# Optimization experiments

Measured on AMD Instinct MI355X. Metric: run time of the kernel, lower is better.

## Reference

```python
import jax, jax.numpy as jnp
import numpy as np

# 4x4 Walsh-Hadamard matrix in natural (Hadamard/Kronecker) order: H4 = H2 (x) H2
_H4 = jnp.array([[1, 1, 1, 1],
                 [1, -1, 1, -1],
                 [1, 1, -1, -1],
                 [1, -1, -1, 1]], dtype=jnp.float32)

T = 16          # number of 2D WHT coefficients (4x4 block)
BLK = 4         # spatial block size


def _iwht_stream(trans, weight):
    """trans: (16, B, nH, nW, C); weight: (16, C, K) -> out: (B, 4*nH, 4*nW, K).

    Per-coefficient channel mixing in the transform domain, then inverse 2D
    Walsh-Hadamard transform (separable, scale 1/16) back to spatial domain.
    """
    _, B, nH, nW, C = trans.shape
    K = weight.shape[2]
    # transform-domain channel mixing: (t,b,h,w,c) x (t,c,k) -> (t,b,h,w,k)
    mixed = jnp.einsum('tbhwc,tck->tbhwk', trans, weight)
    # split coefficient index t = 4*u + v (row/col frequency)
    mixed = mixed.reshape(BLK, BLK, B, nH, nW, K)
    # inverse separable WHT: out[b,nh,i,nw,j,k] = (1/16) sum_{u,v} H4[i,u] H4[j,v] mixed[u,v,...]
    out = jnp.einsum('iu,jv,uvbhwk->bhiwjk', _H4, _H4, mixed) * (1.0 / 16.0)
    return out.reshape(B, nH * BLK, nW * BLK, K)


def setup_inputs() -> dict:
    key = jax.random.key(0)
    k1, k2, k3, k4 = jax.random.split(key, 4)
    B, nH, nW, C = 16, 28, 28, 64
    out_channels = 128
    K1 = out_channels // 2
    K2 = out_channels // 2 + out_channels % 2
    transIm1 = jax.random.normal(k1, (T, B, nH, nW, C), dtype=jnp.float32)
    transIm2 = jax.random.normal(k2, (T, B, nH, nW, C), dtype=jnp.float32)
    weight1 = jax.random.normal(k3, (T, C, K1), dtype=jnp.float32) * 0.02
    weight2 = jax.random.normal(k4, (T, C, K2), dtype=jnp.float32) * 0.02
    bias1 = jnp.zeros((1, 1, 1, K1), dtype=jnp.float32)
    bias2 = jnp.zeros((1, 1, 1, K2), dtype=jnp.float32)
    return {"transIm1": transIm1, "transIm2": transIm2,
            "weight1": weight1, "weight2": weight2,
            "bias1": bias1, "bias2": bias2}


def reference(transIm1, transIm2, weight1, weight2, bias1, bias2):
    out1 = _iwht_stream(transIm1, weight1) + bias1
    out2 = _iwht_stream(transIm2, weight2) + bias2
    return (out1, out2)
```

## Files before the change

kernel.cpp:

```cpp
#include <hip/hip_runtime.h>
#include <hip/hip_bf16.h>

typedef float f32x4 __attribute__((ext_vector_type(4)));
typedef short s16x8 __attribute__((ext_vector_type(8)));

#define NPIX       12544
#define OUT_STRIDE 12845056
#define NTILES     1568
#define GRIDX      512

__device__ __forceinline__ unsigned short f2bf(float x) {
    union { float f; unsigned u; } un; un.f = x;
    unsigned r = un.u + 0x7FFFu + ((un.u >> 16) & 1u);
    return (unsigned short)(r >> 16);
}

__device__ __forceinline__ short bfs(float x) {
    __hip_bfloat16 h = __float2bfloat16(x);
    return *reinterpret_cast<short*>(&h);
}

__device__ __forceinline__ void gload_lds16(const void* g, void* l) {
    __builtin_amdgcn_global_load_lds(
        (const __attribute__((address_space(1))) unsigned int*)g,
        (__attribute__((address_space(3))) unsigned int*)l, 16, 0, 0);
}

__global__ __launch_bounds__(256) void repack_weights(
        const float* __restrict__ w1, const float* __restrict__ w2,
        unsigned short* __restrict__ wf) {
    int gid = blockIdx.x * 256 + threadIdx.x;
    int k = gid & 63;
    int c = (gid >> 6) & 63;
    int t = (gid >> 12) & 15;
    int s = (gid >> 16) & 1;
    const float* __restrict__ w = s ? w2 : w1;
    float val = w[gid & 65535] * 0.0625f;
    int e = c & 7, lhi = (c >> 3) & 3, ks = c >> 5;
    int l  = lhi * 16 + (k & 15);
    int nt = k >> 4;
    int dst = ((((s * 16 + t) * 2 + ks) * 4 + nt) * 64 + l) * 8 + e;
    wf[dst] = f2bf(val);
}

__global__ __launch_bounds__(256, 2) void iwht_main(
        const float* __restrict__ trans1, const float* __restrict__ trans2,
        const unsigned short* __restrict__ wf,
        const float* __restrict__ bias1, const float* __restrict__ bias2,
        float* __restrict__ out) {
    __shared__ __align__(16) unsigned char lds[65536];

    const int tid  = threadIdx.x;
    const int wid  = tid >> 6;
    const int lane = tid & 63;
    const int lrow = lane & 15;
    const int lhi  = lane >> 4;

    const s16x8* __restrict__ wbb = (const s16x8*)wf;

    for (int tau = blockIdx.x; tau < NTILES; tau += GRIDX) {
        const int s   = (tau >= 784) ? 1 : 0;
        const int bid = tau - s * 784;
        const float* __restrict__ trans = s ? trans2 : trans1;
        const int p0 = bid * 16;

        {
            const int ks = wid >> 1, j = wid & 1;
            const float* g0 = trans + (size_t)(p0 + lrow) * 64
                                    + (ks * 8 + lhi * 2 + j) * 4;
            #pragma unroll
            for (int t = 0; t < 16; ++t)
                gload_lds16(g0 + (size_t)t * (NPIX * 64),
                            lds + t * 4096 + wid * 1024);
        }

        const s16x8* __restrict__ wb = wbb + (size_t)s * 8192 + wid * 64 + lane;
        s16x8 bA[8], bB[8];
        #pragma unroll
        for (int v = 0; v < 4; ++v) {
            bA[v]     = wb[(size_t)(v * 8 + 0) * 64];
            bA[4 + v] = wb[(size_t)(v * 8 + 4) * 64];
        }

        f32x4 o[4][4];
        #pragma unroll
        for (int i = 0; i < 4; ++i)
            #pragma unroll
            for (int j = 0; j < 4; ++j)
                o[i][j] = (f32x4){0.f, 0.f, 0.f, 0.f};

        __syncthreads();

        #pragma unroll 1
        for (int uu = 0; uu < 4; uu += 2) {
            #pragma unroll
            for (int v = 0; v < 4; ++v) {
                int t = (uu + 1) * 4 + v;
                bB[v]     = wb[(size_t)(t * 8 + 0) * 64];
                bB[4 + v] = wb[(size_t)(t * 8 + 4) * 64];
            }
            #pragma unroll
            for (int half = 0; half < 2; ++half) {
                const int u = uu + half;
                f32x4 acc[4];
                #pragma unroll
                for (int v = 0; v < 4; ++v) {
                    const int t = u * 4 + v;
                    const unsigned char* ab = lds + t * 4096 + lane * 16;
                    f32x4 q0 = *(const f32x4*)(ab);
                    f32x4 q1 = *(const f32x4*)(ab + 1024);
                    f32x4 q2 = *(const f32x4*)(ab + 2048);
                    f32x4 q3 = *(const f32x4*)(ab + 3072);
                    s16x8 a0, a1;
                    #pragma unroll
                    for (int e = 0; e < 4; ++e) {
                        a0[e] = bfs(q0[e]); a0[4 + e] = bfs(q1[e]);
                        a1[e] = bfs(q2[e]); a1[4 + e] = bfs(q3[e]);
                    }
                    f32x4 tacc = {0.f, 0.f, 0.f, 0.f};
                    if (half == 0) {
                        tacc = __builtin_amdgcn_mfma_f32_16x16x32_bf16(a0, bA[v],     tacc, 0, 0, 0);
                        tacc = __builtin_amdgcn_mfma_f32_16x16x32_bf16(a1, bA[4 + v], tacc, 0, 0, 0);
                    } else {
                        tacc = __builtin_amdgcn_mfma_f32_16x16x32_bf16(a0, bB[v],     tacc, 0, 0, 0);
                        tacc = __builtin_amdgcn_mfma_f32_16x16x32_bf16(a1, bB[4 + v], tacc, 0, 0, 0);
                    }
                    acc[v] = tacc;
                }
                if (half == 0 && uu + 2 < 4) {
                    #pragma unroll
                    for (int v = 0; v < 4; ++v) {
                        int t = (uu + 2) * 4 + v;
                        bA[v]     = wb[(size_t)(t * 8 + 0) * 64];
                        bA[4 + v] = wb[(size_t)(t * 8 + 4) * 64];
                    }
                }
                f32x4 e0 = acc[0] + acc[1], e1 = acc[0] - acc[1];
                f32x4 e2 = acc[2] + acc[3], e3 = acc[2] - acc[3];
                f32x4 g0 = e0 + e2, g1 = e1 + e3, g2 = e0 - e2, g3 = e1 - e3;
                const float s1 = (u & 1) ? -1.f : 1.f;
                const float s2 = (u & 2) ? -1.f : 1.f;
                const float s3 = s1 * s2;
                #pragma unroll
                for (int j = 0; j < 4; ++j) {
                    f32x4 gj = (j == 0) ? g0 : ((j == 1) ? g1 : ((j == 2) ? g2 : g3));
                    o[0][j] += gj;
                    o[1][j] += s1 * gj;
                    o[2][j] += s2 * gj;
                    o[3][j] += s3 * gj;
                }
            }
        }

        const float* __restrict__ bias = s ? bias2 : bias1;
        const int k = wid * 16 + lrow;
        const float bk = bias[k];
        __syncthreads();
        #pragma unroll
        for (int i = 0; i < 4; ++i)
            #pragma unroll
            for (int j = 0; j < 4; ++j)
                #pragma unroll
                for (int r = 0; r < 4; ++r) {
                    int p = lhi * 4 + r;
                    int w = k ^ (4 * (p & 7)) ^ (16 * (j & 1));
                    *(float*)(lds + p * 4096 + i * 1024 + j * 256 + w * 4) = o[i][j][r] + bk;
                }
        __syncthreads();
        const int bimg = bid / 49;
        const int hw0  = (bid % 49) * 16;
        float* __restrict__ outp = out + (s ? (size_t)OUT_STRIDE : 0);
        #pragma unroll
        for (int n = 0; n < 16; ++n) {
            int idx = wid * 16 + n;
            int p = idx >> 2, i = idx & 3;
            int hw = hw0 + p;
            int h = hw / 28, w = hw % 28;
            size_t rowbase = ((size_t)(bimg * 112 + h * 4 + i) * 112 + w * 4) * 64;
            int g = (lane & 15) ^ (p & 7) ^ (4 * ((lane >> 4) & 1));
            f32x4 val = *(const f32x4*)(lds + p * 4096 + i * 1024
                                        + (lane >> 4) * 256 + g * 16);
            *(f32x4*)(outp + rowbase + lane * 4) = val;
        }
        __syncthreads();
    }
}

extern "C" void kernel_launch(void* const* d_in, const int* in_sizes, int n_in,
                              void* d_out, int out_size, void* d_ws, size_t ws_size,
                              hipStream_t stream) {
    const float* t1 = (const float*)d_in[0];
    const float* t2 = (const float*)d_in[1];
    const float* w1 = (const float*)d_in[2];
    const float* w2 = (const float*)d_in[3];
    const float* b1 = (const float*)d_in[4];
    const float* b2 = (const float*)d_in[5];
    unsigned short* wfrag = (unsigned short*)d_ws;
    float* out = (float*)d_out;

    repack_weights<<<dim3(512), dim3(256), 0, stream>>>(w1, w2, wfrag);
    iwht_main<<<dim3(GRIDX), dim3(256), 0, stream>>>(t1, t2, wfrag, b1, b2, out);
}
```

Measured before the change: 202.7 us.

## Double-buffer half-tile input staging and store output directly from registers

The per-tile loop is split into half-tiles of 8 WHT coefficients. Each half is staged into one of two LDS buffers while the previous half is computed, using an explicit vmcnt wait and a raw barrier in place of full __syncthreads. The LDS transpose of the output is removed: each lane writes its accumulated values straight to global memory as scalar stores, with bias values hoisted out of the loop. This aims to hide global load latency and cut LDS round trips and barriers. The cost is many more, narrower store instructions with less coalescing, and weight fragments reloaded for every half.

```diff
diff --git a/kernel.cpp b/kernel.cpp
--- a/kernel.cpp
+++ b/kernel.cpp
@@ -55,134 +55,133 @@
     const int lane = tid & 63;
     const int lrow = lane & 15;
     const int lhi  = lane >> 4;
-
-    const s16x8* __restrict__ wbb = (const s16x8*)wf;
-
-    for (int tau = blockIdx.x; tau < NTILES; tau += GRIDX) {
+    const int bx   = blockIdx.x;
+
+    const int   kk  = wid * 16 + lrow;
+    const float bk1 = bias1[kk];
+    const float bk2 = bias2[kk];
+
+    const int M = ((NTILES - bx + GRIDX - 1) / GRIDX) * 2;
+
+    const int qsrc = (wid >> 1) * 32 + lhi * 8 + (wid & 1) * 4;
+    const s16x8* __restrict__ wbbase = (const s16x8*)wf + (size_t)wid * 64 + lane;
+
+    auto stage_half = [&](int m) {
+        const int tau = bx + (m >> 1) * GRIDX;
+        const int hf  = m & 1;
         const int s   = (tau >= 784) ? 1 : 0;
         const int bid = tau - s * 784;
-        const float* __restrict__ trans = s ? trans2 : trans1;
-        const int p0 = bid * 16;
+        const float* __restrict__ tr = s ? trans2 : trans1;
+        const float* g0 = tr + (size_t)(bid * 16 + lrow) * 64 + qsrc;
+        unsigned char* db = lds + (m & 1) * 32768 + wid * 1024;
+        #pragma unroll
+        for (int tt = 0; tt < 8; ++tt) {
+            const int t = hf * 8 + tt;
+            gload_lds16(g0 + (size_t)t * (NPIX * 64), db + tt * 4096);
+        }
+    };
+
+    f32x4 o[4][4];
+    #pragma unroll
+    for (int i = 0; i < 4; ++i)
+        #pragma unroll
+        for (int j = 0; j < 4; ++j)
+            o[i][j] = (f32x4){0.f, 0.f, 0.f, 0.f};
+
+    s16x8 bH[16];
+
+    stage_half(0);
+
+    #pragma unroll 1
+    for (int m = 0; m < M; ++m) {
+        const int tau = bx + (m >> 1) * GRIDX;
+        const int hf  = m & 1;
+        const int s   = (tau >= 784) ? 1 : 0;
+        const int bid = tau - s * 784;
 
         {
-            const int ks = wid >> 1, j = wid & 1;
-            const float* g0 = trans + (size_t)(p0 + lrow) * 64
-                                    + (ks * 8 + lhi * 2 + j) * 4;
-            #pragma unroll
-            for (int t = 0; t < 16; ++t)
-                gload_lds16(g0 + (size_t)t * (NPIX * 64),
-                            lds + t * 4096 + wid * 1024);
-        }
-
-        const s16x8* __restrict__ wb = wbb + (size_t)s * 8192 + wid * 64 + lane;
-        s16x8 bA[8], bB[8];
+            const s16x8* __restrict__ wb = wbbase + (size_t)s * 8192;
+            #pragma unroll
+            for (int tt = 0; tt < 8; ++tt) {
+                const int t = hf * 8 + tt;
+                bH[tt * 2 + 0] = wb[(size_t)(t * 2 + 0) * 256];
+                bH[tt * 2 + 1] = wb[(size_t)(t * 2 + 1) * 256];
+            }
+        }
+
+        if (m + 1 < M) {
+            stage_half(m + 1);
+            asm volatile("s_waitcnt vmcnt(8)" ::: "memory");
+        } else {
+            asm volatile("s_waitcnt vmcnt(0)" ::: "memory");
+        }
+        __builtin_amdgcn_sched_barrier(0);
+        __builtin_amdgcn_s_barrier();
+
+        const unsigned char* __restrict__ hb = lds + (m & 1) * 32768;
         #pragma unroll
-        for (int v = 0; v < 4; ++v) {
-            bA[v]     = wb[(size_t)(v * 8 + 0) * 64];
-            bA[4 + v] = wb[(size_t)(v * 8 + 4) * 64];
-        }
-
-        f32x4 o[4][4];
-        #pragma unroll
-        for (int i = 0; i < 4; ++i)
-            #pragma unroll
-            for (int j = 0; j < 4; ++j)
-                o[i][j] = (f32x4){0.f, 0.f, 0.f, 0.f};
-
-        __syncthreads();
-
-        #pragma unroll 1
-        for (int uu = 0; uu < 4; uu += 2) {
+        for (int g = 0; g < 2; ++g) {
+            f32x4 acc[4];
             #pragma unroll
             for (int v = 0; v < 4; ++v) {
-                int t = (uu + 1) * 4 + v;
-                bB[v]     = wb[(size_t)(t * 8 + 0) * 64];
-                bB[4 + v] = wb[(size_t)(t * 8 + 4) * 64];
-            }
-            #pragma unroll
-            for (int half = 0; half < 2; ++half) {
-                const int u = uu + half;
-                f32x4 acc[4];
+                const int tt = g * 4 + v;
+                const unsigned char* ab = hb + tt * 4096 + lane * 16;
+                f32x4 q0 = *(const f32x4*)(ab);
+                f32x4 q1 = *(const f32x4*)(ab + 1024);
+                f32x4 q2 = *(const f32x4*)(ab + 2048);
+                f32x4 q3 = *(const f32x4*)(ab + 3072);
+                s16x8 a0, a1;
                 #pragma unroll
-                for (int v = 0; v < 4; ++v) {
-                    const int t = u * 4 + v;
-                    const unsigned char* ab = lds + t * 4096 + lane * 16;
-                    f32x4 q0 = *(const f32x4*)(ab);
-                    f32x4 q1 = *(const f32x4*)(ab + 1024);
-                    f32x4 q2 = *(const f32x4*)(ab + 2048);
-                    f32x4 q3 = *(const f32x4*)(ab + 3072);
-                    s16x8 a0, a1;
-                    #pragma unroll
-                    for (int e = 0; e < 4; ++e) {
-                        a0[e] = bfs(q0[e]); a0[4 + e] = bfs(q1[e]);
-                        a1[e] = bfs(q2[e]); a1[4 + e] = bfs(q3[e]);
-                    }
-                    f32x4 tacc = {0.f, 0.f, 0.f, 0.f};
-                    if (half == 0) {
-                        tacc = __builtin_amdgcn_mfma_f32_16x16x32_bf16(a0, bA[v],     tacc, 0, 0, 0);
-                        tacc = __builtin_amdgcn_mfma_f32_16x16x32_bf16(a1, bA[4 + v], tacc, 0, 0, 0);
-                    } else {
-                        tacc = __builtin_amdgcn_mfma_f32_16x16x32_bf16(a0, bB[v],     tacc, 0, 0, 0);
-                        tacc = __builtin_amdgcn_mfma_f32_16x16x32_bf16(a1, bB[4 + v], tacc, 0, 0, 0);
-                    }
-                    acc[v] = tacc;
+                for (int e = 0; e < 4; ++e) {
+                    a0[e] = bfs(q0[e]); a0[4 + e] = bfs(q1[e]);
+                    a1[e] = bfs(q2[e]); a1[4 + e] = bfs(q3[e]);
                 }
-                if (half == 0 && uu + 2 < 4) {
-                    #pragma unroll
-                    for (int v = 0; v < 4; ++v) {
-                        int t = (uu + 2) * 4 + v;
-                        bA[v]     = wb[(size_t)(t * 8 + 0) * 64];
-                        bA[4 + v] = wb[(size_t)(t * 8 + 4) * 64];
-                    }
-                }
-                f32x4 e0 = acc[0] + acc[1], e1 = acc[0] - acc[1];
-                f32x4 e2 = acc[2] + acc[3], e3 = acc[2] - acc[3];
-                f32x4 g0 = e0 + e2, g1 = e1 + e3, g2 = e0 - e2, g3 = e1 - e3;
-                const float s1 = (u & 1) ? -1.f : 1.f;
-                const float s2 = (u & 2) ? -1.f : 1.f;
-                const float s3 = s1 * s2;
+                f32x4 tacc = {0.f, 0.f, 0.f, 0.f};
+                tacc = __builtin_amdgcn_mfma_f32_16x16x32_bf16(a0, bH[tt * 2 + 0], tacc, 0, 0, 0);
+                tacc = __builtin_amdgcn_mfma_f32_16x16x32_bf16(a1, bH[tt * 2 + 1], tacc, 0, 0, 0);
+                acc[v] = tacc;
+            }
+            f32x4 e0 = acc[0] + acc[1], e1 = acc[0] - acc[1];
+            f32x4 e2 = acc[2] + acc[3], e3 = acc[2] - acc[3];
+            f32x4 g0 = e0 + e2, g1 = e1 + e3, g2 = e0 - e2, g3 = e1 - e3;
+            const int u = hf * 2 + g;
+            const float s1 = (u & 1) ? -1.f : 1.f;
+            const float s2 = (u & 2) ? -1.f : 1.f;
+            const float s3 = s1 * s2;
+            #pragma unroll
+            for (int j = 0; j < 4; ++j) {
+                f32x4 gj = (j == 0) ? g0 : ((j == 1) ? g1 : ((j == 2) ? g2 : g3));
+                o[0][j] += gj;
+                o[1][j] += s1 * gj;
+                o[2][j] += s2 * gj;
+                o[3][j] += s3 * gj;
+            }
+        }
+
+        if (hf) {
+            const float bk = s ? bk2 : bk1;
+            const int bimg = bid / 49;
+            const int hw0  = (bid % 49) * 16;
+            float* __restrict__ outp = out + (s ? (size_t)OUT_STRIDE : 0);
+            size_t rbase[4];
+            #pragma unroll
+            for (int r = 0; r < 4; ++r) {
+                int hw = hw0 + lhi * 4 + r;
+                int h = hw / 28, w = hw % 28;
+                rbase[r] = ((size_t)(bimg * 112 + h * 4) * 112 + (w * 4)) * 64 + kk;
+            }
+            #pragma unroll
+            for (int i = 0; i < 4; ++i)
                 #pragma unroll
                 for (int j = 0; j < 4; ++j) {
-                    f32x4 gj = (j == 0) ? g0 : ((j == 1) ? g1 : ((j == 2) ? g2 : g3));
-                    o[0][j] += gj;
-                    o[1][j] += s1 * gj;
-                    o[2][j] += s2 * gj;
-                    o[3][j] += s3 * gj;
+                    #pragma unroll
+                    for (int r = 0; r < 4; ++r)
+                        outp[rbase[r] + (size_t)((i * 112 + j) * 64)] = o[i][j][r] + bk;
+                    o[i][j] = (f32x4){0.f, 0.f, 0.f, 0.f};
                 }
-            }
-        }
-
-        const float* __restrict__ bias = s ? bias2 : bias1;
-        const int k = wid * 16 + lrow;
-        const float bk = bias[k];
-        __syncthreads();
-        #pragma unroll
-        for (int i = 0; i < 4; ++i)
-            #pragma unroll
-            for (int j = 0; j < 4; ++j)
-                #pragma unroll
-                for (int r = 0; r < 4; ++r) {
-                    int p = lhi * 4 + r;
-                    int w = k ^ (4 * (p & 7)) ^ (16 * (j & 1));
-                    *(float*)(lds + p * 4096 + i * 1024 + j * 256 + w * 4) = o[i][j][r] + bk;
-                }
-        __syncthreads();
-        const int bimg = bid / 49;
-        const int hw0  = (bid % 49) * 16;
-        float* __restrict__ outp = out + (s ? (size_t)OUT_STRIDE : 0);
-        #pragma unroll
-        for (int n = 0; n < 16; ++n) {
-            int idx = wid * 16 + n;
-            int p = idx >> 2, i = idx & 3;
-            int hw = hw0 + p;
-            int h = hw / 28, w = hw % 28;
-            size_t rowbase = ((size_t)(bimg * 112 + h * 4 + i) * 112 + w * 4) * 64;
-            int g = (lane & 15) ^ (p & 7) ^ (4 * ((lane >> 4) & 1));
-            f32x4 val = *(const f32x4*)(lds + p * 4096 + i * 1024
-                                        + (lane >> 4) * 256 + g * 16);
-            *(f32x4*)(outp + rowbase + lane * 4) = val;
-        }
-        __syncthreads();
+        }
+
+        __builtin_amdgcn_s_barrier();
     }
 }
 
```

Measured after the change: 204.8 us. Within noise of the previous version (+1.0%).
